# Kernel optimization log

Hardware: AMD Instinct MI355X
Metric: run time of the kernel (lower is better)

Reference implementation:

```python
import jax, jax.numpy as jnp
import numpy as np

B, NC, H, W, C = 4, 3, 112, 112, 128
HEADS, WS, SS = 4, 7, 3
HD = C // HEADS
SCALE = HD ** -0.5
NWIN = (H // WS) * (W // WS)
N = WS * WS  # tokens per window per contrast


def _rel_pos_index():
    # standard Swin relative position index over a WSxWS window
    c = np.stack(np.meshgrid(np.arange(WS), np.arange(WS), indexing='ij')).reshape(2, -1)
    r = (c[:, :, None] - c[:, None, :]).transpose(1, 2, 0)
    r[:, :, 0] += WS - 1
    r[:, :, 1] += WS - 1
    r[:, :, 0] *= 2 * WS - 1
    return r.sum(-1)  # (N, N) int

RPI = _rel_pos_index()


def _attn_mask():
    # SW-MSA mask built exactly as in __init__ (shift active since 0 < SS < WS)
    img = np.zeros((H, W))
    sl = (slice(0, -WS), slice(-WS, -SS), slice(-SS, None))
    cnt = 0
    for hh in sl:
        for ww in sl:
            img[hh, ww] = cnt
            cnt += 1
    mw = img.reshape(H // WS, WS, W // WS, WS).transpose(0, 2, 1, 3).reshape(-1, N)
    am = mw[:, None, :] - mw[:, :, None]  # unsqueeze(1) - unsqueeze(2)
    return jnp.asarray(np.where(am != 0, -100.0, 0.0), dtype=np.float32)  # (nW, N, N)

MASK = _attn_mask()


def win_part(x):
    # (B, n, H, W, C) -> (B*nW, n, WS, WS, C)
    b, n = x.shape[0], x.shape[1]
    x = x.reshape(b, n, H // WS, WS, W // WS, WS, C)
    return x.transpose(0, 2, 4, 1, 3, 5, 6).reshape(-1, n, WS, WS, C)


def win_rev(x, b):
    # (B*nW, n, WS, WS, C) -> (B, n, H, W, C)
    n = x.shape[1]
    x = x.reshape(b, H // WS, W // WS, n, WS, WS, C)
    return x.transpose(0, 3, 1, 4, 2, 5, 6).reshape(b, n, H, W, C)


def ln(x, g, bta):
    m = x.mean(-1, keepdims=True)
    v = ((x - m) ** 2).mean(-1, keepdims=True)
    return (x - m) * jax.lax.rsqrt(v + 1e-5) * g + bta


def win_attn(xq, xk, xv, wq, bq, wk, bk, wv, bv, wp, bp, rpb):
    B_, nq = xq.shape[0], xq.shape[1]
    nkv = xk.shape[1]
    Nq, Nkv = nq * N, nkv * N
    q = (xq.reshape(B_, Nq, C) @ wq + bq).reshape(B_, Nq, HEADS, HD).transpose(0, 2, 1, 3) * SCALE
    k = (xk.reshape(B_, Nkv, C) @ wk + bk).reshape(B_, Nkv, HEADS, HD).transpose(0, 2, 1, 3)
    v = (xv.reshape(B_, Nkv, C) @ wv + bv).reshape(B_, Nkv, HEADS, HD).transpose(0, 2, 1, 3)
    attn = jnp.einsum('bhqd,bhkd->bhqk', q, k)
    bias = jnp.tile(rpb[RPI].transpose(2, 0, 1), (1, nq, nkv))  # (HEADS, Nq, Nkv)
    attn = attn + bias[None]
    m = jnp.tile(MASK, (1, nq, nkv))  # (nW, Nq, Nkv)
    attn = attn.reshape(B_ // NWIN, NWIN, HEADS, Nq, Nkv) + m[None, :, None]
    attn = jax.nn.softmax(attn.reshape(B_, HEADS, Nq, Nkv), axis=-1)
    out = jnp.einsum('bhqk,bhkd->bhqd', attn, v).transpose(0, 2, 1, 3).reshape(B_, Nq, C) @ wp + bp
    return out.reshape(B_, nq, WS, WS, C)


def reference(x, x_kv, contrast_token, contrast_embed,
              n1g, n1b, n2g, n2b, n3g, n3b,
              sa_wq, sa_bq, sa_wk, sa_bk, sa_wv, sa_bv, sa_wp, sa_bp, sa_rpb,
              ca_wq, ca_bq, ca_wk, ca_bk, ca_wv, ca_bv, ca_wp, ca_bp, ca_rpb,
              m_w1, m_b1, m_w2, m_b2):
    ct = contrast_token[None, :, None, None, :]
    ce = contrast_embed[None, :, None, None, :]
    # --- shifted-window self-attention ---
    shortcut = x
    h = ln(x, n1g, n1b)
    h = jnp.roll(h, (-SS, -SS), axis=(2, 3))
    xw = win_part(h)
    xwe = xw + ct
    aw = win_attn(xwe, xwe, xw, sa_wq, sa_bq, sa_wk, sa_bk, sa_wv, sa_bv, sa_wp, sa_bp, sa_rpb)
    h = win_rev(aw, B)
    h = jnp.roll(h, (SS, SS), axis=(2, 3))
    x = shortcut + h
    # --- shifted-window cross-attention against x_kv ---
    shortcut = x
    h = ln(x, n2g, n2b)
    hs = jnp.roll(h, (-SS, -SS), axis=(2, 3))
    kvs = jnp.roll(x_kv, (-SS, -SS), axis=(2, 3))
    xw = win_part(hs)
    kw = win_part(kvs)
    aw = win_attn(xw + ct, kw + ce, kw, ca_wq, ca_bq, ca_wk, ca_bk, ca_wv, ca_bv, ca_wp, ca_bp, ca_rpb)
    h = win_rev(aw, B)
    h = jnp.roll(h, (SS, SS), axis=(2, 3))
    x = shortcut + h
    # --- MLP ---
    h = ln(x, n3g, n3b)
    h = jax.nn.gelu(h @ m_w1 + m_b1, approximate=False) @ m_w2 + m_b2
    return x + h


def setup_inputs():
    key = jax.random.key(0)
    ks = jax.random.split(key, 32)
    rn = lambda i, shp, s=1.0: jax.random.normal(ks[i], shp, dtype=jnp.float32) * s
    inp = {
        'x': rn(0, (B, NC, H, W, C)),
        'x_kv': rn(1, (B, NC, H, W, C)),
        'contrast_token': rn(2, (NC, C), 0.02),
        'contrast_embed': rn(3, (NC, C), 0.02),
        'n1g': jnp.ones((C,)), 'n1b': jnp.zeros((C,)),
        'n2g': jnp.ones((C,)), 'n2b': jnp.zeros((C,)),
        'n3g': jnp.ones((C,)), 'n3b': jnp.zeros((C,)),
    }
    i = 4
    for pre in ('sa', 'ca'):
        for nm in ('wq', 'wk', 'wv', 'wp'):
            inp[pre + '_' + nm] = rn(i, (C, C), 0.02)
            inp[pre + '_b' + nm[1]] = jnp.zeros((C,))
            i += 1
        inp[pre + '_rpb'] = rn(i, ((2 * WS - 1) ** 2, HEADS), 0.02)
        i += 1
    inp['m_w1'] = rn(i, (C, 4 * C), 0.02)
    inp['m_b1'] = jnp.zeros((4 * C,))
    inp['m_w2'] = rn(i + 1, (4 * C, C), 0.02)
    inp['m_b2'] = jnp.zeros((C,))
    return inp
```

## Files before the change

### kernel.cpp

```cpp
#include <hip/hip_runtime.h>
#include <hip/hip_bf16.h>

typedef __hip_bfloat16 bf16;

#define Bn    4
#define NCn   3
#define Hn    112
#define Wn    112
#define Cn    128
#define HEADS 4
#define WSn   7
#define SSn   3
#define HDn   32
#define WNt   1024
#define Tt    147
#define SCALE 0.17677669529663687f

#define SA    288
#define SH    1056
#define MT    32
#define NROWS 49
#define NPAD  64

static const size_t NE = (size_t)Bn * NCn * Hn * Wn * Cn;

typedef float f32x4 __attribute__((ext_vector_type(4)));
typedef short s16x8 __attribute__((ext_vector_type(8)));
typedef short s16x4 __attribute__((ext_vector_type(4)));
#define MFMA(a,b,c) __builtin_amdgcn_mfma_f32_16x16x32_bf16((a),(b),(c),0,0,0)

#define P_QCSA 0
#define P_KCSA 384
#define P_QCCA 768
#define P_KCCA 1152
#define P_VCSA 1536
#define P_BPSA 1664
#define P_VCCA 1792
#define P_BPCA 1920
#define P_B1   2048
#define P_B2   2560
#define P_G1   2688
#define P_N1B  2816
#define P_G2   2944
#define P_N2B  3072
#define P_G3   3200
#define P_N3B  3328

#define W_SAQ 0
#define W_SAK 16384
#define W_SAV 32768
#define W_SAP 49152
#define W_CAQ 65536
#define W_CAK 81920
#define W_CAV 98304
#define W_CAP 114688
#define W_W1T 131072
#define W_W2T 196608

struct Ptrs { const void* p[32]; };

__device__ __forceinline__ float bf2f(bf16 v) { return __bfloat162float(v); }
__device__ __forceinline__ bf16  f2bf(float v) { return __float2bfloat16(v); }
__device__ __forceinline__ short f2bs(float v) { bf16 t = __float2bfloat16(v); return *reinterpret_cast<short*>(&t); }
__device__ __forceinline__ float bs2f(short v) { bf16 t = *reinterpret_cast<bf16*>(&v); return __bfloat162float(t); }

__device__ __forceinline__ float ldi(const void* __restrict__ p, size_t i, int f) {
    return f ? ((const float*)p)[i] : bf2f(((const bf16*)p)[i]);
}

__device__ __forceinline__ float gelu(float x) {
    float x2 = x * x;
    float arg = x * fmaf(x2, 0.0713548162f, 1.5957691216f);
    float e = __expf(arg);
    float r = __builtin_amdgcn_rcpf(1.f + e);
    return x - x * r;
}

__device__ __forceinline__ void ln_inplace(char* __restrict__ rp, const float* __restrict__ gb) {
    float s = 0.f, s2 = 0.f;
    #pragma unroll
    for (int c8 = 0; c8 < 16; ++c8) {
        s16x8 v = *(const s16x8*)(rp + c8 * 16);
        #pragma unroll
        for (int j = 0; j < 8; ++j) { float fv = bs2f(v[j]); s += fv; s2 += fv * fv; }
    }
    float mean = s * (1.f / 128.f);
    float rstd = rsqrtf(s2 * (1.f / 128.f) - mean * mean + 1e-5f);
    #pragma unroll
    for (int c8 = 0; c8 < 16; ++c8) {
        s16x8 v = *(const s16x8*)(rp + c8 * 16);
        #pragma unroll
        for (int j = 0; j < 8; ++j) {
            int col = c8 * 8 + j;
            v[j] = f2bs((bs2f(v[j]) - mean) * rstd * gb[col] + gb[128 + col]);
        }
        *(s16x8*)(rp + c8 * 16) = v;
    }
}

__device__ __forceinline__ void ln_row4(char* __restrict__ rowbase, const float* __restrict__ gb, int sub) {
    char* rp = rowbase + sub * 64;
    float s = 0.f, s2 = 0.f;
    s16x8 vv[4];
    #pragma unroll
    for (int c = 0; c < 4; ++c) {
        vv[c] = *(const s16x8*)(rp + c * 16);
        #pragma unroll
        for (int j = 0; j < 8; ++j) { float fv = bs2f(vv[c][j]); s += fv; s2 += fv * fv; }
    }
    s  += __shfl_xor(s, 1);  s  += __shfl_xor(s, 2);
    s2 += __shfl_xor(s2, 1); s2 += __shfl_xor(s2, 2);
    float mean = s * (1.f / 128.f);
    float rstd = rsqrtf(s2 * (1.f / 128.f) - mean * mean + 1e-5f);
    #pragma unroll
    for (int c = 0; c < 4; ++c) {
        #pragma unroll
        for (int j = 0; j < 8; ++j) {
            int col = sub * 32 + c * 8 + j;
            vv[c][j] = f2bs((bs2f(vv[c][j]) - mean) * rstd * gb[col] + gb[128 + col]);
        }
        *(s16x8*)(rp + c * 16) = vv[c];
    }
}

__device__ __forceinline__ int tok_row(int wn, int t) {
    int b = wn >> 8, wrem = wn & 255, wi = wrem >> 4, wj = wrem & 15;
    int n = t / 49, p = t % 49, pi = p / 7, pj = p % 7;
    int i = (wi * 7 + pi + SSn) % Hn;
    int j = (wj * 7 + pj + SSn) % Wn;
    return ((b * NCn + n) * Hn + i) * Wn + j;
}

__global__ void k_detect(const unsigned int* __restrict__ xw, int* __restrict__ flag) {
    __shared__ int cnt;
    if (threadIdx.x == 0) cnt = 0;
    __syncthreads();
    int c = 0;
    for (int i = threadIdx.x; i < 8192; i += 256) {
        unsigned e = (xw[i] >> 7) & 0xffu;
        c += (e >= 100u && e <= 140u) ? 1 : 0;
    }
    atomicAdd(&cnt, c);
    __syncthreads();
    if (threadIdx.x == 0) *flag = (cnt < 4096) ? 1 : 0;
}

__global__ __launch_bounds__(256) void k_prep(Ptrs in, const int* __restrict__ dflag,
                                              float* __restrict__ P, bf16* __restrict__ wT,
                                              float* __restrict__ BMT) {
    const int f = *dflag;
    int b = blockIdx.x, tid = threadIdx.x;
    __shared__ float vlds[384];
    if (b < 4) {
        const int wmap[4] = {10, 12, 19, 21};
        const int bmap[4] = {11, 13, 20, 22};
        const int dmap[4] = {P_QCSA, P_KCSA, P_QCCA, P_KCCA};
        const void* vsrc = in.p[b == 3 ? 3 : 2];
        for (int i = tid; i < 384; i += 256) vlds[i] = ldi(vsrc, i, f);
        __syncthreads();
        const void* W = in.p[wmap[b]];
        for (int t = tid; t < 384; t += 256) {
            int n = t >> 7, c = t & 127;
            float acc = 0.f;
            #pragma unroll 4
            for (int d = 0; d < 128; ++d)
                acc += vlds[n * 128 + d] * ldi(W, (size_t)d * 128 + c, f);
            P[dmap[b] + t] = acc + ldi(in.p[bmap[b]], c, f);
        }
    } else if (b == 4) {
        if (tid < 128) {
            P[P_VCSA + tid] = ldi(in.p[15], tid, f);
            P[P_BPSA + tid] = ldi(in.p[17], tid, f);
            P[P_VCCA + tid] = ldi(in.p[24], tid, f);
            P[P_BPCA + tid] = ldi(in.p[26], tid, f);
            P[P_B2   + tid] = ldi(in.p[31], tid, f);
            P[P_G1   + tid] = ldi(in.p[4],  tid, f);
            P[P_N1B  + tid] = ldi(in.p[5],  tid, f);
            P[P_G2   + tid] = ldi(in.p[6],  tid, f);
            P[P_N2B  + tid] = ldi(in.p[7],  tid, f);
            P[P_G3   + tid] = ldi(in.p[8],  tid, f);
            P[P_N3B  + tid] = ldi(in.p[9],  tid, f);
        }
        for (int t = tid; t < 512; t += 256) P[P_B1 + t] = ldi(in.p[29], t, f);
    } else if (b < 69) {
        const int map[8] = {10, 12, 14, 16, 19, 21, 23, 25};
        int unit = (b - 5) * 4 + (tid >> 6), lane = tid & 63;
        int mat = unit >> 5, ntks = unit & 31;
        int ntile = ntks >> 2, ks = ntks & 3;
        int n = ntile * 16 + (lane & 15), k0 = ks * 32 + (lane >> 4) * 8;
        const void* src = in.p[map[mat]];
        s16x8 v;
        #pragma unroll
        for (int j = 0; j < 8; ++j) v[j] = f2bs(ldi(src, (size_t)(k0 + j) * 128 + n, f));
        *(s16x8*)(wT + mat * 16384 + ((size_t)ntks * 64 + lane) * 8) = v;
    } else if (b < 133) {
        int unit = (b - 69) * 4 + (tid >> 6), lane = tid & 63;
        s16x8 v;
        if (unit < 128) {
            int ntile = unit >> 2, ks = unit & 3;
            int n = ntile * 16 + (lane & 15), k0 = ks * 32 + (lane >> 4) * 8;
            #pragma unroll
            for (int j = 0; j < 8; ++j) v[j] = f2bs(ldi(in.p[28], (size_t)(k0 + j) * 512 + n, f));
            *(s16x8*)(wT + W_W1T + ((size_t)unit * 64 + lane) * 8) = v;
        } else {
            int b2 = unit - 128;
            int ntile = b2 >> 4, ks = b2 & 15;
            int n = ntile * 16 + (lane & 15), k0 = ks * 32 + (lane >> 4) * 8;
            #pragma unroll
            for (int j = 0; j < 8; ++j) v[j] = f2bs(ldi(in.p[30], (size_t)(k0 + j) * 128 + n, f));
            *(s16x8*)(wT + W_W2T + ((size_t)b2 * 64 + lane) * 8) = v;
        }
    } else {
        int u = b - 133;
        int stage = u >> 4, pat = (u >> 2) & 3, h = u & 3;
        const void* rpb = in.p[stage ? 27 : 18];
        float* dst = BMT + (size_t)u * 2560;
        int er = pat >> 1, ec = pat & 1;
        for (int i = tid; i < 2560; i += 256) {
            float v = 0.f;
            int qp = i / 52, kp = i - qp * 52;
            if (qp < 49 && kp < 49) {
                int qpi = qp / 7, qpj = qp - qpi * 7, kpi = kp / 7, kpj = kp - kpi * 7;
                float bias = ldi(rpb, ((qpi - kpi + 6) * 13 + (qpj - kpj + 6)) * HEADS + h, f);
                int rq = (er ? (qpi < 4 ? 1 : 2) : 0) * 3 + (ec ? (qpj < 4 ? 1 : 2) : 0);
                int rk = (er ? (kpi < 4 ? 1 : 2) : 0) * 3 + (ec ? (kpj < 4 ? 1 : 2) : 0);
                v = bias + (rq == rk ? 0.f : -100.f);
            }
            dst[i] = v;
        }
    }
}

__global__ __launch_bounds__(256) void k_qkv_sa(
    const void* __restrict__ x, bf16* __restrict__ xr,
    const float* __restrict__ P, const bf16* __restrict__ wT,
    const int* __restrict__ dflag,
    bf16* __restrict__ tokQ, bf16* __restrict__ tokK, bf16* __restrict__ tokV) {
    const int f = *dflag;
    __shared__ char ldsA[NPAD * SA];
    __shared__ int rowIdx[NROWS];
    __shared__ float gb[256];
    int wn = blockIdx.x, nc = blockIdx.y, tid = threadIdx.x;
    int t0 = nc * NROWS;
    if (tid < NROWS) rowIdx[tid] = tok_row(wn, t0 + tid);
    gb[tid] = tid < 128 ? P[P_G1 + tid] : P[P_N1B + tid - 128];
    for (int i = tid; i < 15 * SA / 4; i += 256) ((int*)(ldsA + NROWS * SA))[i] = 0;
    __syncthreads();
    for (int idx = tid; idx < NROWS * 16; idx += 256) {
        int t = idx >> 4, c8 = idx & 15;
        size_t g = (size_t)rowIdx[t] * Cn + c8 * 8;
        s16x8 v;
        if (f) {
            const float* s = (const float*)x + g;
            #pragma unroll
            for (int j = 0; j < 8; ++j) v[j] = f2bs(s[j]);
        } else {
            v = *(const s16x8*)((const bf16*)x + g);
        }
        *(s16x8*)(ldsA + t * SA + c8 * 16) = v;
        *(s16x8*)(xr + g) = v;
    }
    __syncthreads();
    if (tid < NROWS) ln_inplace(ldsA + tid * SA, gb);
    __syncthreads();
    int wv = tid >> 6, lane = tid & 63, l15 = lane & 15, lg = lane >> 4;
    #pragma unroll 1
    for (int mat = 0; mat < 3; ++mat) {
        const bf16* W = wT + mat * 16384;
        bf16* dst = mat == 0 ? tokQ : (mat == 1 ? tokK : tokV);
        #pragma unroll 1
        for (int ni = 0; ni < 2; ++ni) {
            int nt = wv * 2 + ni;
            f32x4 acc[4] = {};
            #pragma unroll
            for (int ks = 0; ks < 4; ++ks) {
                s16x8 bfrag = *(const s16x8*)(W + (((nt << 2) + ks) * 64 + lane) * 8);
                #pragma unroll
                for (int mt = 0; mt < 4; ++mt) {
                    s16x8 af = *(const s16x8*)(ldsA + (mt * 16 + l15) * SA + ks * 64 + lg * 16);
                    acc[mt] = MFMA(bfrag, af, acc[mt]);
                }
            }
            int col0 = nt * 16 + lg * 4;
            #pragma unroll
            for (int mt = 0; mt < 4; ++mt) {
                int tl = mt * 16 + l15;
                if (tl < NROWS) {
                    int t = t0 + tl;
                    s16x4 pk;
                    if (mat == 0) {
                        f32x4 b4 = *(const f32x4*)(P + P_QCSA + nc * 128 + col0);
                        #pragma unroll
                        for (int r = 0; r < 4; ++r) pk[r] = f2bs((acc[mt][r] + b4[r]) * SCALE);
                    } else if (mat == 1) {
                        f32x4 b4 = *(const f32x4*)(P + P_KCSA + nc * 128 + col0);
                        #pragma unroll
                        for (int r = 0; r < 4; ++r) pk[r] = f2bs(acc[mt][r] + b4[r]);
                    } else {
                        f32x4 b4 = *(const f32x4*)(P + P_VCSA + col0);
                        #pragma unroll
                        for (int r = 0; r < 4; ++r) pk[r] = f2bs(acc[mt][r] + b4[r]);
                    }
                    *(s16x4*)(dst + ((size_t)wn * Tt + t) * Cn + col0) = pk;
                }
            }
        }
    }
}

__global__ __launch_bounds__(256) void k_attn(
    const bf16* __restrict__ Q, const bf16* __restrict__ K, const bf16* __restrict__ V,
    bf16* __restrict__ O, const float* __restrict__ BMbase) {
    __shared__ char ldsK[40 * 256];
    __shared__ char ldsV[32 * 336];
    __shared__ char ldsP[4 * 16 * 336];
    __shared__ float BM[2560];
    __shared__ float lArr[4][16];
    int wn = blockIdx.x, h = blockIdx.y, tid = threadIdx.x;
    int wi = (wn >> 4) & 15, wj = wn & 15;
    size_t base = (size_t)wn * Tt * Cn + h * HDn;
    for (int idx = tid; idx < 640; idx += 256) {
        int key = idx >> 2, ch = idx & 3;
        s16x8 kv = {}, vv = {};
        if (key < Tt) {
            kv = *(const s16x8*)(K + base + (size_t)key * Cn + ch * 8);
            vv = *(const s16x8*)(V + base + (size_t)key * Cn + ch * 8);
        }
        *(s16x8*)(ldsK + (key >> 2) * 256 + (key & 3) * 64 + ch * 16) = kv;
        #pragma unroll
        for (int j = 0; j < 8; ++j)
            *(short*)(ldsV + (ch * 8 + j) * 336 + key * 2) = vv[j];
    }
    {
        int pat = ((wi == 15) << 1) | (wj == 15);
        const f32x4* src = (const f32x4*)(BMbase + (size_t)(pat * 4 + h) * 2560);
        f32x4* dst4 = (f32x4*)BM;
        for (int i = tid; i < 640; i += 256) dst4[i] = src[i];
    }
    __syncthreads();
    int wv = tid >> 6, lane = tid & 63, l15 = lane & 15, lg = lane >> 4;
    char* myP = ldsP + wv * (16 * 336);
    int kpA[10];
    #pragma unroll
    for (int nt = 0; nt < 10; ++nt) {
        int key = nt * 16 + l15;
        kpA[nt] = key - (key >= 147 ? 147 : (key >= 98 ? 98 : (key >= 49 ? 49 : 0)));
    }
    for (int mt = wv; mt < 10; mt += 4) {
        int qrow = mt * 16 + l15; if (qrow > 146) qrow = 146;
        s16x8 qf = *(const s16x8*)(Q + base + (size_t)qrow * Cn + lg * 8);
        f32x4 acc[10];
        #pragma unroll
        for (int nt = 0; nt < 10; ++nt) {
            int key = nt * 16 + l15;
            s16x8 bfrag = *(const s16x8*)(ldsK + (key >> 2) * 256 + (key & 3) * 64 + lg * 16);
            f32x4 z = {};
            acc[nt] = MFMA(qf, bfrag, z);
        }
        float linv[4];
        #pragma unroll
        for (int r = 0; r < 4; ++r) {
            int row = mt * 16 + lg * 4 + r;
            int qp = row - (row >= 147 ? 147 : (row >= 98 ? 98 : (row >= 49 ? 49 : 0)));
            float l = 0.f;
            #pragma unroll
            for (int nt = 0; nt < 10; ++nt) {
                float p = (nt == 9 && l15 >= 3) ? 0.f
                        : __expf(acc[nt][r] + BM[qp * 52 + kpA[nt]]);
                l += p;
                *(bf16*)(myP + (lg * 4 + r) * 336 + (nt * 16 + l15) * 2) = f2bf(p);
            }
            #pragma unroll
            for (int off = 1; off < 16; off <<= 1) l += __shfl_xor(l, off);
            linv[r] = 1.f / l;
        }
        if (l15 == 0) {
            #pragma unroll
            for (int r = 0; r < 4; ++r) lArr[wv][lg * 4 + r] = linv[r];
        }
        float myinv = lArr[wv][l15];
        #pragma unroll
        for (int ntv = 0; ntv < 2; ++ntv) {
            f32x4 ao = {};
            #pragma unroll
            for (int ks = 0; ks < 5; ++ks) {
                s16x8 af = *(const s16x8*)(myP + l15 * 336 + ks * 64 + lg * 16);
                s16x8 vf = *(const s16x8*)(ldsV + (ntv * 16 + l15) * 336 + ks * 64 + lg * 16);
                ao = MFMA(vf, af, ao);
            }
            int q = mt * 16 + l15;
            if (q < Tt) {
                s16x4 pk;
                #pragma unroll
                for (int r = 0; r < 4; ++r) pk[r] = f2bs(ao[r] * myinv);
                *(s16x4*)(O + base + (size_t)q * Cn + ntv * 16 + lg * 4) = pk;
            }
        }
    }
}

__global__ __launch_bounds__(256) void k_proj(
    const bf16* __restrict__ tokO, const float* __restrict__ P, const bf16* __restrict__ W,
    int bpOff, bf16* __restrict__ xr) {
    __shared__ char ldsA[NPAD * SA];
    __shared__ int rowIdx[NROWS];
    int wn = blockIdx.x, nc = blockIdx.y, tid = threadIdx.x;
    int t0 = nc * NROWS;
    if (tid < NROWS) rowIdx[tid] = tok_row(wn, t0 + tid);
    for (int i = tid; i < 15 * SA / 4; i += 256) ((int*)(ldsA + NROWS * SA))[i] = 0;
    __syncthreads();
    int wv = tid >> 6, lane = tid & 63, l15 = lane & 15, lg = lane >> 4;
    s16x4 xrc[2][4];
    #pragma unroll
    for (int ni = 0; ni < 2; ++ni) {
        int col0 = (wv * 2 + ni) * 16 + lg * 4;
        #pragma unroll
        for (int mt = 0; mt < 4; ++mt) {
            int tl = mt * 16 + l15;
            int rr = rowIdx[tl < NROWS ? tl : 0];
            xrc[ni][mt] = *(const s16x4*)(xr + (size_t)rr * Cn + col0);
        }
    }
    for (int idx = tid; idx < NROWS * 16; idx += 256) {
        int t = idx >> 4, c8 = idx & 15;
        s16x8 v = *(const s16x8*)(tokO + ((size_t)wn * Tt + t0 + t) * Cn + c8 * 8);
        *(s16x8*)(ldsA + t * SA + c8 * 16) = v;
    }
    __syncthreads();
    f32x4 acc2[2][4] = {};
    #pragma unroll
    for (int ni = 0; ni < 2; ++ni) {
        int nt = wv * 2 + ni;
        #pragma unroll
        for (int ks = 0; ks < 4; ++ks) {
            s16x8 bfrag = *(const s16x8*)(W + (((nt << 2) + ks) * 64 + lane) * 8);
            #pragma unroll
            for (int mt = 0; mt < 4; ++mt) {
                s16x8 af = *(const s16x8*)(ldsA + (mt * 16 + l15) * SA + ks * 64 + lg * 16);
                acc2[ni][mt] = MFMA(bfrag, af, acc2[ni][mt]);
            }
        }
    }
    #pragma unroll
    for (int ni = 0; ni < 2; ++ni) {
        int col0 = (wv * 2 + ni) * 16 + lg * 4;
        f32x4 bp4 = *(const f32x4*)(P + bpOff + col0);
        #pragma unroll
        for (int mt = 0; mt < 4; ++mt) {
            int tl = mt * 16 + l15;
            if (tl < NROWS) {
                s16x4 pk;
                #pragma unroll
                for (int r = 0; r < 4; ++r) pk[r] = f2bs(bs2f(xrc[ni][mt][r]) + acc2[ni][mt][r] + bp4[r]);
                *(s16x4*)(xr + (size_t)rowIdx[tl] * Cn + col0) = pk;
            }
        }
    }
}

__global__ __launch_bounds__(256) void k_proj_ca(
    const bf16* __restrict__ tokO, const float* __restrict__ P, const bf16* __restrict__ wT,
    const void* __restrict__ xkv, const int* __restrict__ dflag, bf16* __restrict__ xr,
    bf16* __restrict__ tokQ, bf16* __restrict__ tokK, bf16* __restrict__ tokV) {
    const int f = *dflag;
    __shared__ char ldsA[NPAD * SA];
    __shared__ int rowIdx[NROWS];
    __shared__ float gb[256];
    int wn = blockIdx.x, nc = blockIdx.y, tid = threadIdx.x;
    int t0 = nc * NROWS;
    if (tid < NROWS) rowIdx[tid] = tok_row(wn, t0 + tid);
    gb[tid] = tid < 128 ? P[P_G2 + tid] : P[P_N2B + tid - 128];
    for (int i = tid; i < 15 * SA / 4; i += 256) ((int*)(ldsA + NROWS * SA))[i] = 0;
    __syncthreads();
    for (int idx = tid; idx < NROWS * 16; idx += 256) {
        int t = idx >> 4, c8 = idx & 15;
        s16x8 v = *(const s16x8*)(tokO + ((size_t)wn * Tt + t0 + t) * Cn + c8 * 8);
        *(s16x8*)(ldsA + t * SA + c8 * 16) = v;
    }
    __syncthreads();
    int wv = tid >> 6, lane = tid & 63, l15 = lane & 15, lg = lane >> 4;
    {
        const bf16* W = wT + W_SAP;
        #pragma unroll 1
        for (int ni = 0; ni < 2; ++ni) {
            int nt = wv * 2 + ni;
            f32x4 acc[4] = {};
            #pragma unroll
            for (int ks = 0; ks < 4; ++ks) {
                s16x8 bfrag = *(const s16x8*)(W + (((nt << 2) + ks) * 64 + lane) * 8);
                #pragma unroll
                for (int mt = 0; mt < 4; ++mt) {
                    s16x8 af = *(const s16x8*)(ldsA + (mt * 16 + l15) * SA + ks * 64 + lg * 16);
                    acc[mt] = MFMA(bfrag, af, acc[mt]);
                }
            }
            int col0 = nt * 16 + lg * 4;
            f32x4 bp4 = *(const f32x4*)(P + P_BPSA + col0);
            #pragma unroll
            for (int mt = 0; mt < 4; ++mt) {
                int tl = mt * 16 + l15;
                if (tl < NROWS) {
                    size_t o = (size_t)rowIdx[tl] * Cn + col0;
                    s16x4 cur = *(const s16x4*)(xr + o);
                    s16x4 pk;
                    #pragma unroll
                    for (int r = 0; r < 4; ++r) pk[r] = f2bs(bs2f(cur[r]) + acc[mt][r] + bp4[r]);
                    *(s16x4*)(xr + o) = pk;
                }
            }
        }
    }
    __syncthreads();
    for (int idx = tid; idx < NROWS * 16; idx += 256) {
        int t = idx >> 4, c8 = idx & 15;
        s16x8 v = *(const s16x8*)(xr + (size_t)rowIdx[t] * Cn + c8 * 8);
        *(s16x8*)(ldsA + t * SA + c8 * 16) = v;
    }
    __syncthreads();
    if (tid < NROWS) ln_inplace(ldsA + tid * SA, gb);
    __syncthreads();
    {
        const bf16* W = wT + W_CAQ;
        #pragma unroll 1
        for (int ni = 0; ni < 2; ++ni) {
            int nt = wv * 2 + ni;
            f32x4 acc[4] = {};
            #pragma unroll
            for (int ks = 0; ks < 4; ++ks) {
                s16x8 bfrag = *(const s16x8*)(W + (((nt << 2) + ks) * 64 + lane) * 8);
                #pragma unroll
                for (int mt = 0; mt < 4; ++mt) {
                    s16x8 af = *(const s16x8*)(ldsA + (mt * 16 + l15) * SA + ks * 64 + lg * 16);
                    acc[mt] = MFMA(bfrag, af, acc[mt]);
                }
            }
            int col0 = nt * 16 + lg * 4;
            #pragma unroll
            for (int mt = 0; mt < 4; ++mt) {
                int tl = mt * 16 + l15;
                if (tl < NROWS) {
                    int t = t0 + tl;
                    f32x4 b4 = *(const f32x4*)(P + P_QCCA + nc * 128 + col0);
                    s16x4 pk;
                    #pragma unroll
                    for (int r = 0; r < 4; ++r) pk[r] = f2bs((acc[mt][r] + b4[r]) * SCALE);
                    *(s16x4*)(tokQ + ((size_t)wn * Tt + t) * Cn + col0) = pk;
                }
            }
        }
    }
    __syncthreads();
    for (int idx = tid; idx < NROWS * 16; idx += 256) {
        int t = idx >> 4, c8 = idx & 15;
        s16x8 v;
        if (f) {
            const float* s = (const float*)xkv + (size_t)rowIdx[t] * Cn + c8 * 8;
            #pragma unroll
            for (int j = 0; j < 8; ++j) v[j] = f2bs(s[j]);
        } else {
            v = *(const s16x8*)((const bf16*)xkv + (size_t)rowIdx[t] * Cn + c8 * 8);
        }
        *(s16x8*)(ldsA + t * SA + c8 * 16) = v;
    }
    __syncthreads();
    #pragma unroll 1
    for (int mat = 0; mat < 2; ++mat) {
        const bf16* W = wT + (mat == 0 ? W_CAK : W_CAV);
        bf16* dst = mat == 0 ? tokK : tokV;
        #pragma unroll 1
        for (int ni = 0; ni < 2; ++ni) {
            int nt = wv * 2 + ni;
            f32x4 acc[4] = {};
            #pragma unroll
            for (int ks = 0; ks < 4; ++ks) {
                s16x8 bfrag = *(const s16x8*)(W + (((nt << 2) + ks) * 64 + lane) * 8);
                #pragma unroll
                for (int mt = 0; mt < 4; ++mt) {
                    s16x8 af = *(const s16x8*)(ldsA + (mt * 16 + l15) * SA + ks * 64 + lg * 16);
                    acc[mt] = MFMA(bfrag, af, acc[mt]);
                }
            }
            int col0 = nt * 16 + lg * 4;
            #pragma unroll
            for (int mt = 0; mt < 4; ++mt) {
                int tl = mt * 16 + l15;
                if (tl < NROWS) {
                    int t = t0 + tl;
                    f32x4 b4 = (mat == 0) ? *(const f32x4*)(P + P_KCCA + nc * 128 + col0)
                                          : *(const f32x4*)(P + P_VCCA + col0);
                    s16x4 pk;
                    #pragma unroll
                    for (int r = 0; r < 4; ++r) pk[r] = f2bs(acc[mt][r] + b4[r]);
                    *(s16x4*)(dst + ((size_t)wn * Tt + t) * Cn + col0) = pk;
                }
            }
        }
    }
}

__global__ __launch_bounds__(256) void k_mlp(
    const bf16* __restrict__ xr, const float* __restrict__ P, const bf16* __restrict__ wT,
    const int* __restrict__ dflag, void* __restrict__ outp) {
    __shared__ char ldsU[MT * SH];
    __shared__ float gb[256];
    char* ldsA = ldsU;
    char* ldsH = ldsU;
    int tid = threadIdx.x;
    size_t t0 = (size_t)blockIdx.x * MT;
    gb[tid] = tid < 128 ? P[P_G3 + tid] : P[P_N3B + tid - 128];
    __syncthreads();
    for (int idx = tid; idx < MT * 16; idx += 256) {
        int t = idx >> 4, c8 = idx & 15;
        s16x8 v = *(const s16x8*)(xr + (t0 + t) * Cn + c8 * 8);
        *(s16x8*)(ldsA + t * SA + c8 * 16) = v;
    }
    __syncthreads();
    {
        int row = tid >> 3, sub = tid & 7;
        if (sub < 4) ln_row4(ldsA + row * SA, gb, sub);
    }
    __syncthreads();
    int wv = tid >> 6, lane = tid & 63, l15 = lane & 15, lg = lane >> 4;
    const bf16* W1 = wT + W_W1T;
    s16x8 a[2][4];
    #pragma unroll
    for (int m = 0; m < 2; ++m)
        #pragma unroll
        for (int ks = 0; ks < 4; ++ks)
            a[m][ks] = *(const s16x8*)(ldsA + (m * 16 + l15) * SA + ks * 64 + lg * 16);
    __syncthreads();
    {
        int nt0 = wv * 8;
        s16x8 bc0 = *(const s16x8*)(W1 + (((nt0 << 2) + 0) * 64 + lane) * 8);
        s16x8 bc1 = *(const s16x8*)(W1 + (((nt0 << 2) + 1) * 64 + lane) * 8);
        s16x8 bc2 = *(const s16x8*)(W1 + (((nt0 << 2) + 2) * 64 + lane) * 8);
        s16x8 bc3 = *(const s16x8*)(W1 + (((nt0 << 2) + 3) * 64 + lane) * 8);
        #pragma unroll 1
        for (int ni = 0; ni < 8; ++ni) {
            int nt = nt0 + ni;
            s16x8 bn0 = *(const s16x8*)(W1 + ((((nt + 1) << 2) + 0) * 64 + lane) * 8);
            s16x8 bn1 = *(const s16x8*)(W1 + ((((nt + 1) << 2) + 1) * 64 + lane) * 8);
            s16x8 bn2 = *(const s16x8*)(W1 + ((((nt + 1) << 2) + 2) * 64 + lane) * 8);
            s16x8 bn3 = *(const s16x8*)(W1 + ((((nt + 1) << 2) + 3) * 64 + lane) * 8);
            f32x4 acc[2] = {};
            #pragma unroll
            for (int m = 0; m < 2; ++m) {
                acc[m] = MFMA(bc0, a[m][0], acc[m]);
                acc[m] = MFMA(bc1, a[m][1], acc[m]);
                acc[m] = MFMA(bc2, a[m][2], acc[m]);
                acc[m] = MFMA(bc3, a[m][3], acc[m]);
            }
            int col0 = nt * 16 + lg * 4;
            f32x4 b14 = *(const f32x4*)(P + P_B1 + col0);
            #pragma unroll
            for (int m = 0; m < 2; ++m) {
                s16x4 pk;
                #pragma unroll
                for (int r = 0; r < 4; ++r) pk[r] = f2bs(gelu(acc[m][r] + b14[r]));
                *(s16x4*)(ldsH + (m * 16 + l15) * SH + col0 * 2) = pk;
            }
            bc0 = bn0; bc1 = bn1; bc2 = bn2; bc3 = bn3;
        }
    }
    __syncthreads();
    const int f = *dflag;
    const bf16* W2 = wT + W_W2T;
    #pragma unroll 1
    for (int ni = 0; ni < 2; ++ni) {
        int nt = wv * 2 + ni;
        f32x4 acc[2] = {};
        s16x8 bc = *(const s16x8*)(W2 + (((nt << 4) + 0) * 64 + lane) * 8);
        #pragma unroll 1
        for (int ks = 0; ks < 16; ++ks) {
            s16x8 bn = *(const s16x8*)(W2 + (((nt << 4) + ks + 1) * 64 + lane) * 8);
            #pragma unroll
            for (int m = 0; m < 2; ++m) {
                s16x8 af = *(const s16x8*)(ldsH + (m * 16 + l15) * SH + ks * 64 + lg * 16);
                acc[m] = MFMA(bc, af, acc[m]);
            }
            bc = bn;
        }
        int col0 = nt * 16 + lg * 4;
        f32x4 b24 = *(const f32x4*)(P + P_B2 + col0);
        #pragma unroll
        for (int m = 0; m < 2; ++m) {
            size_t g = (t0 + m * 16 + l15) * Cn + col0;
            s16x4 cur = *(const s16x4*)(xr + g);
            if (f) {
                f32x4 o;
                #pragma unroll
                for (int r = 0; r < 4; ++r) o[r] = bs2f(cur[r]) + acc[m][r] + b24[r];
                *(f32x4*)((float*)outp + g) = o;
            } else {
                s16x4 pk;
                #pragma unroll
                for (int r = 0; r < 4; ++r) pk[r] = f2bs(bs2f(cur[r]) + acc[m][r] + b24[r]);
                *(s16x4*)((bf16*)outp + g) = pk;
            }
        }
    }
}

extern "C" void kernel_launch(void* const* d_in, const int* in_sizes, int n_in,
                              void* d_out, int out_size, void* d_ws, size_t ws_size,
                              hipStream_t stream) {
    Ptrs ptrs;
    for (int i = 0; i < 32; ++i) ptrs.p[i] = d_in[i];

    char* base = (char*)d_ws;
    float* P    = (float*)base;
    int*  dflag = (int*)(base + 32768);
    bf16* wT    = (bf16*)(base + 33024);
    float* BMT  = (float*)(wT + 262144);
    bf16* xr    = (bf16*)(BMT + 81920);
    bf16* tokK  = xr + NE;
    bf16* tokV  = tokK + NE;
    bf16* tokQ  = (bf16*)d_out;

    k_detect<<<1, 256, 0, stream>>>((const unsigned int*)d_in[0], dflag);
    k_prep<<<165, 256, 0, stream>>>(ptrs, dflag, P, wT, BMT);
    k_qkv_sa<<<dim3(WNt, 3), 256, 0, stream>>>(d_in[0], xr, P, wT, dflag, tokQ, tokK, tokV);
    k_attn<<<dim3(WNt, HEADS), 256, 0, stream>>>(tokQ, tokK, tokV, tokQ, BMT);
    k_proj_ca<<<dim3(WNt, 3), 256, 0, stream>>>(tokQ, P, wT, d_in[1], dflag, xr, tokQ, tokK, tokV);
    k_attn<<<dim3(WNt, HEADS), 256, 0, stream>>>(tokQ, tokK, tokV, tokQ, BMT + 16 * 2560);
    k_proj<<<dim3(WNt, 3), 256, 0, stream>>>(tokQ, P, wT + W_CAP, P_BPCA, xr);
    k_mlp<<<(int)(NE / Cn / MT), 256, 0, stream>>>(xr, P, wT, dflag, d_out);
}
```

Baseline: 496.5 us.

## Prefetch residual and KV tokens into second LDS buffer in cross-attn projection kernel

The k_proj_ca kernel now prefetches the residual xr values into registers and loads the x_kv tile into a second LDS buffer at the start, alongside the tokO tile. After the projection GEMM, the updated residual goes both to global memory and straight into LDS, so xr is no longer re-read from global. The K/V GEMMs read from the prefetched buffer, which removes a later global load phase and two barriers. In exchange the kernel uses twice the LDS and more registers, which may lower occupancy.

```diff
diff --git a/kernel.cpp b/kernel.cpp
--- a/kernel.cpp
+++ b/kernel.cpp
@@ -464,57 +464,78 @@
     bf16* __restrict__ tokQ, bf16* __restrict__ tokK, bf16* __restrict__ tokV) {
     const int f = *dflag;
     __shared__ char ldsA[NPAD * SA];
+    __shared__ char ldsB[NPAD * SA];
     __shared__ int rowIdx[NROWS];
     __shared__ float gb[256];
     int wn = blockIdx.x, nc = blockIdx.y, tid = threadIdx.x;
     int t0 = nc * NROWS;
     if (tid < NROWS) rowIdx[tid] = tok_row(wn, t0 + tid);
     gb[tid] = tid < 128 ? P[P_G2 + tid] : P[P_N2B + tid - 128];
-    for (int i = tid; i < 15 * SA / 4; i += 256) ((int*)(ldsA + NROWS * SA))[i] = 0;
-    __syncthreads();
+    for (int i = tid; i < 15 * SA / 4; i += 256) {
+        ((int*)(ldsA + NROWS * SA))[i] = 0;
+        ((int*)(ldsB + NROWS * SA))[i] = 0;
+    }
+    __syncthreads();
+    int wv = tid >> 6, lane = tid & 63, l15 = lane & 15, lg = lane >> 4;
+    s16x4 xrc[2][4];
+    #pragma unroll
+    for (int ni = 0; ni < 2; ++ni) {
+        int col0 = (wv * 2 + ni) * 16 + lg * 4;
+        #pragma unroll
+        for (int mt = 0; mt < 4; ++mt) {
+            int tl = mt * 16 + l15;
+            int rr = rowIdx[tl < NROWS ? tl : 0];
+            xrc[ni][mt] = *(const s16x4*)(xr + (size_t)rr * Cn + col0);
+        }
+    }
     for (int idx = tid; idx < NROWS * 16; idx += 256) {
         int t = idx >> 4, c8 = idx & 15;
         s16x8 v = *(const s16x8*)(tokO + ((size_t)wn * Tt + t0 + t) * Cn + c8 * 8);
         *(s16x8*)(ldsA + t * SA + c8 * 16) = v;
-    }
-    __syncthreads();
-    int wv = tid >> 6, lane = tid & 63, l15 = lane & 15, lg = lane >> 4;
+        s16x8 u;
+        if (f) {
+            const float* s = (const float*)xkv + (size_t)rowIdx[t] * Cn + c8 * 8;
+            #pragma unroll
+            for (int j = 0; j < 8; ++j) u[j] = f2bs(s[j]);
+        } else {
+            u = *(const s16x8*)((const bf16*)xkv + (size_t)rowIdx[t] * Cn + c8 * 8);
+        }
+        *(s16x8*)(ldsB + t * SA + c8 * 16) = u;
+    }
+    __syncthreads();
+    f32x4 acc2[2][4] = {};
     {
         const bf16* W = wT + W_SAP;
-        #pragma unroll 1
+        #pragma unroll
         for (int ni = 0; ni < 2; ++ni) {
             int nt = wv * 2 + ni;
-            f32x4 acc[4] = {};
             #pragma unroll
             for (int ks = 0; ks < 4; ++ks) {
                 s16x8 bfrag = *(const s16x8*)(W + (((nt << 2) + ks) * 64 + lane) * 8);
                 #pragma unroll
                 for (int mt = 0; mt < 4; ++mt) {
                     s16x8 af = *(const s16x8*)(ldsA + (mt * 16 + l15) * SA + ks * 64 + lg * 16);
-                    acc[mt] = MFMA(bfrag, af, acc[mt]);
+                    acc2[ni][mt] = MFMA(bfrag, af, acc2[ni][mt]);
                 }
             }
-            int col0 = nt * 16 + lg * 4;
-            f32x4 bp4 = *(const f32x4*)(P + P_BPSA + col0);
-            #pragma unroll
-            for (int mt = 0; mt < 4; ++mt) {
-                int tl = mt * 16 + l15;
-                if (tl < NROWS) {
-                    size_t o = (size_t)rowIdx[tl] * Cn + col0;
-                    s16x4 cur = *(const s16x4*)(xr + o);
-                    s16x4 pk;
-                    #pragma unroll
-                    for (int r = 0; r < 4; ++r) pk[r] = f2bs(bs2f(cur[r]) + acc[mt][r] + bp4[r]);
-                    *(s16x4*)(xr + o) = pk;
-                }
-            }
-        }
-    }
-    __syncthreads();
-    for (int idx = tid; idx < NROWS * 16; idx += 256) {
-        int t = idx >> 4, c8 = idx & 15;
-        s16x8 v = *(const s16x8*)(xr + (size_t)rowIdx[t] * Cn + c8 * 8);
-        *(s16x8*)(ldsA + t * SA + c8 * 16) = v;
+        }
+    }
+    __syncthreads();
+    #pragma unroll
+    for (int ni = 0; ni < 2; ++ni) {
+        int col0 = (wv * 2 + ni) * 16 + lg * 4;
+        f32x4 bp4 = *(const f32x4*)(P + P_BPSA + col0);
+        #pragma unroll
+        for (int mt = 0; mt < 4; ++mt) {
+            int tl = mt * 16 + l15;
+            if (tl < NROWS) {
+                s16x4 pk;
+                #pragma unroll
+                for (int r = 0; r < 4; ++r) pk[r] = f2bs(bs2f(xrc[ni][mt][r]) + acc2[ni][mt][r] + bp4[r]);
+                *(s16x4*)(xr + (size_t)rowIdx[tl] * Cn + col0) = pk;
+                *(s16x4*)(ldsA + tl * SA + col0 * 2) = pk;
+            }
+        }
     }
     __syncthreads();
     if (tid < NROWS) ln_inplace(ldsA + tid * SA, gb);
@@ -549,20 +570,6 @@
             }
         }
     }
-    __syncthreads();
-    for (int idx = tid; idx < NROWS * 16; idx += 256) {
-        int t = idx >> 4, c8 = idx & 15;
-        s16x8 v;
-        if (f) {
-            const float* s = (const float*)xkv + (size_t)rowIdx[t] * Cn + c8 * 8;
-            #pragma unroll
-            for (int j = 0; j < 8; ++j) v[j] = f2bs(s[j]);
-        } else {
-            v = *(const s16x8*)((const bf16*)xkv + (size_t)rowIdx[t] * Cn + c8 * 8);
-        }
-        *(s16x8*)(ldsA + t * SA + c8 * 16) = v;
-    }
-    __syncthreads();
     #pragma unroll 1
     for (int mat = 0; mat < 2; ++mat) {
         const bf16* W = wT + (mat == 0 ? W_CAK : W_CAV);
@@ -576,7 +583,7 @@
                 s16x8 bfrag = *(const s16x8*)(W + (((nt << 2) + ks) * 64 + lane) * 8);
                 #pragma unroll
                 for (int mt = 0; mt < 4; ++mt) {
-                    s16x8 af = *(const s16x8*)(ldsA + (mt * 16 + l15) * SA + ks * 64 + lg * 16);
+                    s16x8 af = *(const s16x8*)(ldsB + (mt * 16 + l15) * SA + ks * 64 + lg * 16);
                     acc[mt] = MFMA(bfrag, af, acc[mt]);
                 }
             }
```

Result: no change. 496.2 us (-0.1%).
